# Performance work log

Measured on AMD Instinct MI355X. Metric: run time of the kernel, lower is better.

Reference implementation:

```python
import jax, jax.numpy as jnp
import numpy as np

B, N, E, P, NH = 8, 1024, 768, 768, 12
HD = P // NH


def setup_inputs() -> dict:
    key = jax.random.key(0)
    ks = jax.random.split(key, 9)
    s = lambda k, sh: jax.random.normal(k, sh, dtype=jnp.float32) * 0.02
    return {
        "x": jax.random.normal(ks[0], (B, N, E), dtype=jnp.float32),
        "wq": s(ks[1], (E, P)), "bq": jnp.zeros((P,), jnp.float32),
        "wk": s(ks[2], (E, P)), "bk": jnp.zeros((P,), jnp.float32),
        "wv": s(ks[3], (E, P)), "bv": jnp.zeros((P,), jnp.float32),
        "wo": s(ks[4], (P, E)), "bo": jnp.zeros((E,), jnp.float32),
        "H": 32, "W": 32,
    }


def reference(x, wq, bq, wk, bk, wv, bv, wo, bo, H, W):
    b, n, _ = x.shape
    # QKV projections: [B,N,P] -> [B,NH,N,HD]
    def split_heads(t):
        return t.reshape(b, n, NH, HD).transpose(0, 2, 1, 3)
    q = split_heads(x @ wq + bq)
    k = split_heads(x @ wk + bk)
    v = split_heads(x @ wv + bv)
    # NOTE: original module applies NO 1/sqrt(head_dim) scaling.
    logits = jnp.einsum("bhqd,bhkd->bhqk", q, k)  # [B,NH,N,N]
    attn = jax.nn.softmax(logits, axis=-1)
    ctx = jnp.einsum("bhqk,bhkd->bhqd", attn, v)  # [B,NH,N,HD]
    ctx = ctx.transpose(0, 2, 1, 3).reshape(b, n, P)
    return ctx @ wo + bo
```

## Files before the change

kernel.cpp:

```cpp
#include <hip/hip_runtime.h>
#include <hip/hip_bf16.h>
#include <math.h>

#define B_   8
#define N_   1024
#define E_   768
#define P_   768
#define NH_  12
#define HD_  64

typedef __attribute__((ext_vector_type(8))) short short8;
typedef __attribute__((ext_vector_type(4))) float f32x4;

__device__ inline void async16(void* lds, const void* g) {
    __builtin_amdgcn_global_load_lds(
        (const __attribute__((address_space(1))) void*)g,
        (__attribute__((address_space(3))) void*)lds, 16, 0, 0);
}

__device__ inline unsigned lds_addr(const void* p) {
    return (unsigned)(unsigned long long)(__attribute__((address_space(3))) const char*)p;
}

__device__ inline unsigned pkbf(float a, float b) {
    union { float f; unsigned u; } ua, ub;
    ua.f = a; ub.f = b;
    return __builtin_amdgcn_perm(ub.u, ua.u, 0x07060302u);
}

__global__ __launch_bounds__(256) void cvt_x(const float* __restrict__ x,
                                             __hip_bfloat16* __restrict__ xb, int n4) {
    int i = blockIdx.x * blockDim.x + threadIdx.x;
    const int stride = gridDim.x * blockDim.x;
    for (; i < n4; i += stride) {
        float4 f = ((const float4*)x)[i];
        union { __hip_bfloat16 h[4]; uint2 u; } pk;
        pk.h[0] = __float2bfloat16(f.x);
        pk.h[1] = __float2bfloat16(f.y);
        pk.h[2] = __float2bfloat16(f.z);
        pk.h[3] = __float2bfloat16(f.w);
        ((uint2*)xb)[i] = pk.u;
    }
}

__global__ __launch_bounds__(256) void cvt_tw(
    const float* __restrict__ W0, const float* __restrict__ W1,
    const float* __restrict__ W2, const float* __restrict__ W3,
    __hip_bfloat16* __restrict__ T0, __hip_bfloat16* __restrict__ T1,
    __hip_bfloat16* __restrict__ T2, __hip_bfloat16* __restrict__ T3) {
    const int z = blockIdx.z;
    const float* W = (z == 0) ? W0 : (z == 1) ? W1 : (z == 2) ? W2 : W3;
    __hip_bfloat16* T = (z == 0) ? T0 : (z == 1) ? T1 : (z == 2) ? T2 : T3;
    __shared__ float t[32][33];
    const int tx = threadIdx.x & 31, ty = threadIdx.x >> 5;
    const int n0 = blockIdx.x * 32, k0 = blockIdx.y * 32;
#pragma unroll
    for (int rr = 0; rr < 4; ++rr)
        t[ty + rr * 8][tx] = W[(k0 + ty + rr * 8) * 768 + n0 + tx];
    __syncthreads();
#pragma unroll
    for (int rr = 0; rr < 4; ++rr)
        T[(long)(n0 + ty + rr * 8) * 768 + k0 + tx] = __float2bfloat16(t[tx][ty + rr * 8]);
}

__global__ __launch_bounds__(512, 2) void gemm256(
    const __hip_bfloat16* __restrict__ A0, const __hip_bfloat16* __restrict__ A1,
    const __hip_bfloat16* __restrict__ A2,
    const __hip_bfloat16* __restrict__ B01, const __hip_bfloat16* __restrict__ B2,
    const float* __restrict__ b0, const float* __restrict__ b1,
    const float* __restrict__ b2,
    void* __restrict__ C0, void* __restrict__ C1, void* __restrict__ C2,
    int fused) {
    constexpr int NT = 12;
    __shared__ char L[9 * 16384];

    const __hip_bfloat16* Arows;
    const __hip_bfloat16* Brows;
    const float* bias;
    void* Cout;
    int mode, rb, cb;
    const int xcd = blockIdx.x & 7, t = blockIdx.x >> 3;
    if (fused) {
        const int g = t % 9, yh = t / 9;
        const int y = yh * 8 + xcd;
        if (g < 6) {
            mode = 2;
            const int z = g / 3;
            rb = (g % 3) * 256; cb = y * 256;
            Arows = z ? A1 : A0; Brows = B01; bias = z ? b1 : b0; Cout = z ? C1 : C0;
        } else {
            mode = 1;
            rb = y * 256; cb = (g - 6) * 256;
            Arows = A2; Brows = B2; bias = b2; Cout = C2;
        }
    } else {
        mode = 3;
        const int e3 = t % 3, yh = t / 3;
        const int y = yh * 8 + xcd;
        rb = e3 * 256; cb = y * 256;
        Arows = A0; Brows = B01; bias = b0; Cout = C0;
    }

    const int tid = threadIdx.x;
    const int lane = tid & 63, w = tid >> 6;
    const int wr = w >> 2, wc = w & 3;
    const int l15 = lane & 15, quad = lane >> 4;

    const int rowoff = tid >> 3;
    const int cchunk = (tid & 7) ^ (rowoff & 7);
    const __hip_bfloat16* pA = Arows + (long)(rb + rowoff) * 768 + cchunk * 8;
    const __hip_bfloat16* pB = Brows + (long)(cb + rowoff) * 768 + cchunk * 8;

    const unsigned ldsB = lds_addr(L);

    const int swz = l15 & 7;
    const unsigned lane0 = (unsigned)(l15 * 128 + ((quad ^ swz) << 4));
    const unsigned lane1 = (unsigned)(l15 * 128 + (((4 + quad) ^ swz) << 4));

#define STG(P_, HF_, KT_, SL_)                                                     \
    do {                                                                           \
        const __hip_bfloat16* s_ = (P_) + (HF_) * (128 * 768) + (KT_) * 64;        \
        async16((char*)L + (SL_) * 16384 + tid * 16, s_);                          \
        async16((char*)L + (SL_) * 16384 + 8192 + tid * 16, s_ + 64 * 768);        \
    } while (0)

    STG(pA, 0, 0, 0);
    STG(pB, 0, 0, 1);
    STG(pB, 1, 0, 2);
    STG(pA, 1, 0, 3);
    STG(pA, 0, 1, 4);

    f32x4 acc[8][4];
#pragma unroll
    for (int i = 0; i < 8; ++i)
#pragma unroll
        for (int j = 0; j < 4; ++j) acc[i][j] = (f32x4){0.f, 0.f, 0.f, 0.f};

    int rs = 0;
    int ss = 5;
    const int sAoff = wr ? 3 : 0;
    const int sBoff = (wc < 2) ? 1 : 2;
    const unsigned bColOff = (unsigned)((wc & 1) * 8192);

    for (int kt = 0; kt < NT; ++kt) {
        if (kt < NT - 1) asm volatile("s_waitcnt vmcnt(2)" ::: "memory");
        else             asm volatile("s_waitcnt vmcnt(0)" ::: "memory");
        int sA = rs + sAoff; if (sA >= 9) sA -= 9;
        int sB = rs + sBoff; if (sB >= 9) sB -= 9;
        const unsigned aBase = ldsB + (unsigned)sA * 16384u;
        const unsigned bBase = ldsB + (unsigned)sB * 16384u + bColOff;

        short8 aF[4][2];
#pragma unroll
        for (int s = 0; s < 4; ++s) {
            __builtin_amdgcn_s_barrier();
            asm volatile("" ::: "memory");
            if (4 * kt + 5 + s < 4 * NT) {
                const int ktile = (4 * kt + 5 + s) >> 2;
                if (s == 0)      STG(pB, 0, ktile, ss);
                else if (s == 1) STG(pB, 1, ktile, ss);
                else if (s == 2) STG(pA, 1, ktile, ss);
                else             STG(pA, 0, ktile, ss);
                ++ss; if (ss == 9) ss = 0;
            }

            const int rh = s >> 1, ch = s & 1;
            if ((s & 1) == 0) {
                const unsigned a0 = aBase + (unsigned)(rh * 8192) + lane0;
                const unsigned a1 = aBase + (unsigned)(rh * 8192) + lane1;
#pragma unroll
                for (int rf = 0; rf < 4; ++rf) {
                    asm volatile("ds_read_b128 %0, %1 offset:%2" : "=v"(aF[rf][0]) : "v"(a0), "i"(rf * 2048));
                    asm volatile("ds_read_b128 %0, %1 offset:%2" : "=v"(aF[rf][1]) : "v"(a1), "i"(rf * 2048));
                }
            }
            short8 bF[2][2];
            {
                const unsigned bb0 = bBase + (unsigned)(ch * 4096) + lane0;
                const unsigned bb1 = bBase + (unsigned)(ch * 4096) + lane1;
#pragma unroll
                for (int cf = 0; cf < 2; ++cf) {
                    asm volatile("ds_read_b128 %0, %1 offset:%2" : "=v"(bF[cf][0]) : "v"(bb0), "i"(cf * 2048));
                    asm volatile("ds_read_b128 %0, %1 offset:%2" : "=v"(bF[cf][1]) : "v"(bb1), "i"(cf * 2048));
                }
            }
            asm volatile("s_waitcnt lgkmcnt(0)" ::: "memory");
            __builtin_amdgcn_sched_barrier(0);
            __builtin_amdgcn_s_setprio(1);
#pragma unroll
            for (int rf = 0; rf < 4; ++rf)
#pragma unroll
                for (int cf = 0; cf < 2; ++cf) {
                    acc[rh * 4 + rf][ch * 2 + cf] = __builtin_amdgcn_mfma_f32_16x16x32_bf16(
                        aF[rf][0], bF[cf][0], acc[rh * 4 + rf][ch * 2 + cf], 0, 0, 0);
                    acc[rh * 4 + rf][ch * 2 + cf] = __builtin_amdgcn_mfma_f32_16x16x32_bf16(
                        aF[rf][1], bF[cf][1], acc[rh * 4 + rf][ch * 2 + cf], 0, 0, 0);
                }
            __builtin_amdgcn_s_setprio(0);
        }
        rs += 4; if (rs >= 9) rs -= 9;
    }
#undef STG

    const int eR = rb + wr * 128;
    const int eC = cb + wc * 64;
    if (mode == 2) {
        __hip_bfloat16* O = (__hip_bfloat16*)Cout;
#pragma unroll
        for (int j = 0; j < 4; ++j) {
            const int n = eC + j * 16 + l15;
            const int bb = n >> 10, nn = n & 1023;
#pragma unroll
            for (int i = 0; i < 8; ++i) {
                const int p0 = eR + i * 16 + quad * 4;
                const int h = p0 >> 6, d0 = p0 & 63;
                const float4 bv = *(const float4*)(bias + p0);
                union { __hip_bfloat16 h4[4]; unsigned long long u; } pk;
                pk.h4[0] = __float2bfloat16(acc[i][j][0] + bv.x);
                pk.h4[1] = __float2bfloat16(acc[i][j][1] + bv.y);
                pk.h4[2] = __float2bfloat16(acc[i][j][2] + bv.z);
                pk.h4[3] = __float2bfloat16(acc[i][j][3] + bv.w);
                *(unsigned long long*)(O + (((long)(bb * NH_ + h)) * N_ + nn) * HD_ + d0) = pk.u;
            }
        }
    } else if (mode == 1) {
        __hip_bfloat16* O = (__hip_bfloat16*)Cout;
#pragma unroll
        for (int j = 0; j < 4; ++j) {
            const int p = eC + j * 16 + l15;
            const int h = p >> 6, d = p & 63;
            const float bv = bias[p];
#pragma unroll
            for (int i = 0; i < 8; ++i) {
                const int n0 = eR + i * 16 + quad * 4;
                const int bb = n0 >> 10, nn = n0 & 1023;
                union { __hip_bfloat16 h4[4]; unsigned long long u; } pk;
#pragma unroll
                for (int r = 0; r < 4; ++r)
                    pk.h4[r] = __float2bfloat16(acc[i][j][r] + bv);
                *(unsigned long long*)(O + (((long)(bb * NH_ + h)) * HD_ + d) * N_ + nn) = pk.u;
            }
        }
    } else {
        float* O = (float*)Cout;
#pragma unroll
        for (int j = 0; j < 4; ++j) {
            const int n = eC + j * 16 + l15;
#pragma unroll
            for (int i = 0; i < 8; ++i) {
                const int e0 = eR + i * 16 + quad * 4;
                const float4 bv = *(const float4*)(bias + e0);
                float4 vo;
                vo.x = acc[i][j][0] + bv.x;
                vo.y = acc[i][j][1] + bv.y;
                vo.z = acc[i][j][2] + bv.z;
                vo.w = acc[i][j][3] + bv.w;
                *(float4*)(O + (long)n * 768 + e0) = vo;
            }
        }
    }
}

__global__ __launch_bounds__(256, 3) void attn_mfma(
    const __hip_bfloat16* __restrict__ Q, const __hip_bfloat16* __restrict__ K,
    const __hip_bfloat16* __restrict__ Vt, __hip_bfloat16* __restrict__ ctx) {
    __shared__ __hip_bfloat16 Ks[3 * 64 * 64];
    __shared__ __hip_bfloat16 Vs[3 * 64 * 64];

    const int tid = threadIdx.x;
    const int lane = tid & 63, w = tid >> 6;
    const int l15 = lane & 15, quad = lane >> 4;
    const int y3 = l15 & 7;

    const int bx = blockIdx.x;
    const int rr_ = bx & 7, t_ = bx >> 3;
    const int qb = t_ & 7, hi_ = t_ >> 3;
    const int H = hi_ * 8 + rr_;
    const int bz = H / 12, hy = H - bz * 12;
    const long headOff = (long)H * (N_ * HD_);
    const int qBase = qb * 128;

    short8 qf[2][2];
#pragma unroll
    for (int i = 0; i < 2; ++i)
#pragma unroll
        for (int ks = 0; ks < 2; ++ks)
            qf[i][ks] = *(const short8*)(Q + headOff +
                (long)(qBase + w * 32 + i * 16 + l15) * HD_ + ks * 32 + quad * 8);
    asm volatile("" :: "v"(qf[0][0]), "v"(qf[0][1]), "v"(qf[1][0]), "v"(qf[1][1]));

    f32x4 o[4][2];
#pragma unroll
    for (int mt = 0; mt < 4; ++mt)
#pragma unroll
        for (int i = 0; i < 2; ++i) o[mt][i] = (f32x4){0.f, 0.f, 0.f, 0.f};
    f32x4 ol[2];
    ol[0] = (f32x4){0.f, 0.f, 0.f, 0.f};
    ol[1] = (f32x4){0.f, 0.f, 0.f, 0.f};
    const short8 onesv = (short8){0x3F80, 0x3F80, 0x3F80, 0x3F80,
                                  0x3F80, 0x3F80, 0x3F80, 0x3F80};

    const int p0 = tid, p1 = tid + 256;
    const int r0 = p0 >> 3, lc0 = (p0 & 7) ^ (r0 & 7);
    const int r1 = p1 >> 3, lc1 = (p1 & 7) ^ (r1 & 7);
    const __hip_bfloat16* gK0 = K + headOff + r0 * HD_ + lc0 * 8;
    const __hip_bfloat16* gK1 = K + headOff + r1 * HD_ + lc1 * 8;
    const __hip_bfloat16* gV0 = Vt + headOff + r0 * N_ + lc0 * 8;
    const __hip_bfloat16* gV1 = Vt + headOff + r1 * N_ + lc1 * 8;
    const int q0 = p0 * 16, q1 = p1 * 16;

    const unsigned kfB0 = lds_addr(Ks) + (unsigned)(l15 * 128 + (((0 * 4 + quad) ^ y3) * 16));
    const unsigned kfB1 = lds_addr(Ks) + (unsigned)(l15 * 128 + (((1 * 4 + quad) ^ y3) * 16));
    unsigned vbB[2][2];
#pragma unroll
    for (int g = 0; g < 2; ++g)
#pragma unroll
        for (int h = 0; h < 2; ++h)
            vbB[g][h] = lds_addr(Vs) + (unsigned)(l15 * 128 +
                (((g * 4 + h * 2 + (quad >> 1)) ^ y3) * 16 + (quad & 1) * 8));

    async16((char*)Ks + q0, gK0);
    async16((char*)Ks + q1, gK1);
    async16((char*)Vs + q0, gV0);
    async16((char*)Vs + q1, gV1);
    async16((char*)Ks + 8192 + q0, gK0 + (long)64 * HD_);
    async16((char*)Ks + 8192 + q1, gK1 + (long)64 * HD_);
    async16((char*)Vs + 8192 + q0, gV0 + 64);
    async16((char*)Vs + 8192 + q1, gV1 + 64);

    for (int it = 0; it < 16; ++it) {
        const int bo = (it % 3) * 8192;
        if (it < 15) asm volatile("s_waitcnt vmcnt(4)" ::: "memory");
        else         asm volatile("s_waitcnt vmcnt(0)" ::: "memory");
        __builtin_amdgcn_s_barrier();
        asm volatile("" ::: "memory");
        if (it + 2 < 16) {
            const int po = ((it + 2) % 3) * 8192;
            const long j1 = (long)(it + 2) * 64;
            async16((char*)Ks + po + q0, gK0 + j1 * HD_);
            async16((char*)Ks + po + q1, gK1 + j1 * HD_);
            async16((char*)Vs + po + q0, gV0 + j1);
            async16((char*)Vs + po + q1, gV1 + j1);
        }

        short8 kf[2][4];
        {
            const unsigned ka0 = kfB0 + bo, ka1 = kfB1 + bo;
#pragma unroll
            for (int n = 0; n < 4; ++n)
                asm volatile("ds_read_b128 %0, %1 offset:%2" : "=v"(kf[0][n]) : "v"(ka0), "i"(n * 2048));
#pragma unroll
            for (int n = 0; n < 4; ++n)
                asm volatile("ds_read_b128 %0, %1 offset:%2" : "=v"(kf[1][n]) : "v"(ka1), "i"(n * 2048));
        }
        f32x4 sT[4][2];
#pragma unroll
        for (int n = 0; n < 4; ++n)
#pragma unroll
            for (int i = 0; i < 2; ++i) sT[n][i] = (f32x4){0.f, 0.f, 0.f, 0.f};
        asm volatile("s_waitcnt lgkmcnt(4)" ::: "memory");
        __builtin_amdgcn_sched_barrier(0);
        __builtin_amdgcn_s_setprio(1);
#pragma unroll
        for (int n = 0; n < 4; ++n)
#pragma unroll
            for (int i = 0; i < 2; ++i)
                sT[n][i] = __builtin_amdgcn_mfma_f32_16x16x32_bf16(kf[0][n], qf[i][0], sT[n][i], 0, 0, 0);
        __builtin_amdgcn_s_setprio(0);
        asm volatile("s_waitcnt lgkmcnt(0)" ::: "memory");
        __builtin_amdgcn_sched_barrier(0);
        __builtin_amdgcn_s_setprio(1);
#pragma unroll
        for (int n = 0; n < 4; ++n)
#pragma unroll
            for (int i = 0; i < 2; ++i)
                sT[n][i] = __builtin_amdgcn_mfma_f32_16x16x32_bf16(kf[1][n], qf[i][1], sT[n][i], 0, 0, 0);
        __builtin_amdgcn_s_setprio(0);

        long v0[4][2];
#pragma unroll
        for (int mt = 0; mt < 4; ++mt)
#pragma unroll
            for (int h = 0; h < 2; ++h)
                asm volatile("ds_read_b64 %0, %1 offset:%2" : "=v"(v0[mt][h]) : "v"(vbB[0][h] + bo), "i"(mt * 2048));

        short8 pf[2][2];
#pragma unroll
        for (int i = 0; i < 2; ++i) {
            float pv[4][4];
#pragma unroll
            for (int n = 0; n < 4; ++n)
#pragma unroll
                for (int r = 0; r < 4; ++r)
                    pv[n][r] = __expf(sT[n][i][r] - 16.635532333438686f);
            union { unsigned u[4]; short8 v; } pk0, pk1;
            pk0.u[0] = pkbf(pv[0][0], pv[0][1]);
            pk0.u[1] = pkbf(pv[0][2], pv[0][3]);
            pk0.u[2] = pkbf(pv[1][0], pv[1][1]);
            pk0.u[3] = pkbf(pv[1][2], pv[1][3]);
            pk1.u[0] = pkbf(pv[2][0], pv[2][1]);
            pk1.u[1] = pkbf(pv[2][2], pv[2][3]);
            pk1.u[2] = pkbf(pv[3][0], pv[3][1]);
            pk1.u[3] = pkbf(pv[3][2], pv[3][3]);
            pf[i][0] = pk0.v;
            pf[i][1] = pk1.v;
        }

        asm volatile("s_waitcnt lgkmcnt(0)" ::: "memory");
        __builtin_amdgcn_sched_barrier(0);
        __builtin_amdgcn_s_setprio(1);
#pragma unroll
        for (int mt = 0; mt < 4; ++mt) {
            union { long l[2]; short8 v; } vb;
            vb.l[0] = v0[mt][0]; vb.l[1] = v0[mt][1];
#pragma unroll
            for (int i = 0; i < 2; ++i)
                o[mt][i] = __builtin_amdgcn_mfma_f32_16x16x32_bf16(vb.v, pf[i][0], o[mt][i], 0, 0, 0);
        }
#pragma unroll
        for (int i = 0; i < 2; ++i)
            ol[i] = __builtin_amdgcn_mfma_f32_16x16x32_bf16(onesv, pf[i][0], ol[i], 0, 0, 0);
        __builtin_amdgcn_s_setprio(0);

        long v1[4][2];
#pragma unroll
        for (int mt = 0; mt < 4; ++mt)
#pragma unroll
            for (int h = 0; h < 2; ++h)
                asm volatile("ds_read_b64 %0, %1 offset:%2" : "=v"(v1[mt][h]) : "v"(vbB[1][h] + bo), "i"(mt * 2048));
        asm volatile("s_waitcnt lgkmcnt(0)" ::: "memory");
        __builtin_amdgcn_sched_barrier(0);
        __builtin_amdgcn_s_setprio(1);
#pragma unroll
        for (int mt = 0; mt < 4; ++mt) {
            union { long l[2]; short8 v; } vb;
            vb.l[0] = v1[mt][0]; vb.l[1] = v1[mt][1];
#pragma unroll
            for (int i = 0; i < 2; ++i)
                o[mt][i] = __builtin_amdgcn_mfma_f32_16x16x32_bf16(vb.v, pf[i][1], o[mt][i], 0, 0, 0);
        }
#pragma unroll
        for (int i = 0; i < 2; ++i)
            ol[i] = __builtin_amdgcn_mfma_f32_16x16x32_bf16(onesv, pf[i][1], ol[i], 0, 0, 0);
        __builtin_amdgcn_s_setprio(0);
    }

#pragma unroll
    for (int i = 0; i < 2; ++i) {
        const float inv = 1.0f / ol[i][0];
        const int q = qBase + w * 32 + i * 16 + l15;
        __hip_bfloat16* op = ctx + ((long)(bz * N_ + q)) * P_ + hy * HD_;
#pragma unroll
        for (int mt = 0; mt < 4; ++mt) {
            union { __hip_bfloat16 h[4]; unsigned long long u; } pk;
#pragma unroll
            for (int r = 0; r < 4; ++r)
                pk.h[r] = __float2bfloat16(o[mt][i][r] * inv);
            *(unsigned long long*)(op + mt * 16 + quad * 4) = pk.u;
        }
    }
}

extern "C" void kernel_launch(void* const* d_in, const int* in_sizes, int n_in,
                              void* d_out, int out_size, void* d_ws, size_t ws_size,
                              hipStream_t stream) {
    const float* x  = (const float*)d_in[0];
    const float* wq = (const float*)d_in[1];
    const float* bq = (const float*)d_in[2];
    const float* wk = (const float*)d_in[3];
    const float* bk = (const float*)d_in[4];
    const float* wv = (const float*)d_in[5];
    const float* bv = (const float*)d_in[6];
    const float* wo = (const float*)d_in[7];
    const float* bo = (const float*)d_in[8];
    float* out = (float*)d_out;

    char* p = (char*)d_ws;
    const long XB = (long)B_ * N_ * E_ * 2;
    const long WB = (long)E_ * P_ * 2;
    const long HB = (long)B_ * NH_ * N_ * HD_ * 2;
    __hip_bfloat16* xb  = (__hip_bfloat16*)p; p += XB;
    __hip_bfloat16* wqt = (__hip_bfloat16*)p; p += WB;
    __hip_bfloat16* wkt = (__hip_bfloat16*)p; p += WB;
    __hip_bfloat16* wvt = (__hip_bfloat16*)p; p += WB;
    __hip_bfloat16* wot = (__hip_bfloat16*)p; p += WB;
    __hip_bfloat16* qh  = (__hip_bfloat16*)p; p += HB;
    __hip_bfloat16* kh  = (__hip_bfloat16*)p; p += HB;
    __hip_bfloat16* vth = (__hip_bfloat16*)p; p += HB;
    __hip_bfloat16* ctxb = (__hip_bfloat16*)p; p += HB;

    cvt_x<<<2048, 256, 0, stream>>>(x, xb, (B_ * N_ * E_) / 4);
    cvt_tw<<<dim3(24, 24, 4), 256, 0, stream>>>(wq, wk, wv, wo, wqt, wkt, wvt, wot);

    gemm256<<<dim3(288), 512, 0, stream>>>(
        wqt, wkt, xb, xb, wvt, bq, bk, bv, qh, kh, vth, 1);

    attn_mfma<<<dim3(768), 256, 0, stream>>>(qh, kh, vth, ctxb);

    gemm256<<<dim3(96), 512, 0, stream>>>(
        wot, wot, xb, ctxb, ctxb, bo, bo, bo, out, out, out, 0);
}
```

Measured before the change: 220.6 us.

## Replace fused QKV projection with smaller-tile triple-buffered 128x128 GEMM kernel

Adds a templated gemm_core kernel that uses 128x128 tiles, 256 threads, a K step of 32 and a three-stage async LDS pipeline, and uses it for the fused Q/K/V projection in place of the 256-tile 512-thread gemm256. The grid grows from 288 to 1152 blocks, which improves load balance and occupancy across CUs. In exchange, each tile reuses its operands less and the kernel has more barriers per K step. The output projection still uses gemm256.

```diff
diff --git a/kernel.cpp b/kernel.cpp
--- a/kernel.cpp
+++ b/kernel.cpp
@@ -61,6 +61,181 @@
 #pragma unroll
     for (int rr = 0; rr < 4; ++rr)
         T[(long)(n0 + ty + rr * 8) * 768 + k0 + tx] = __float2bfloat16(t[tx][ty + rr * 8]);
+}
+
+template <int NC>
+__global__ __launch_bounds__(256) void gemm_core(
+    const __hip_bfloat16* __restrict__ A0, const __hip_bfloat16* __restrict__ A1,
+    const __hip_bfloat16* __restrict__ A2,
+    const __hip_bfloat16* __restrict__ B01, const __hip_bfloat16* __restrict__ B2,
+    const float* __restrict__ b0, const float* __restrict__ b1,
+    const float* __restrict__ b2,
+    void* __restrict__ C0, void* __restrict__ C1, void* __restrict__ C2,
+    int fused) {
+    constexpr int ABUF = 8192;
+    constexpr int BBUF = NC * 64;
+    constexpr int JT = NC / 32;
+    __shared__ char As[3 * ABUF];
+    __shared__ char Bs[3 * BBUF];
+
+    const __hip_bfloat16* Arows;
+    const __hip_bfloat16* Brows;
+    const float* bias;
+    void* Cout;
+    int mode, rb, cb;
+    if (fused) {
+        const int xcd = blockIdx.x & 7, t = blockIdx.x >> 3;
+        const int g = t % 18, yhi = t / 18;
+        const int y = yhi * 8 + xcd;
+        if (g < 12) {
+            mode = 2;
+            const int z = g / 6;
+            rb = (g % 6) * 128; cb = y * 128;
+            Arows = z ? A1 : A0; Brows = B01; bias = z ? b1 : b0; Cout = z ? C1 : C0;
+        } else {
+            mode = 1;
+            rb = y * 128; cb = (g - 12) * 128;
+            Arows = A2; Brows = B2; bias = b2; Cout = C2;
+        }
+    } else {
+        mode = 3;
+        const int xcd = blockIdx.x & 7, t = blockIdx.x >> 3;
+        const int e = t % 6, thi = t / 6;
+        const int tc = thi * 8 + xcd;
+        rb = e * 128; cb = tc * NC;
+        Arows = A0; Brows = B01; bias = b0; Cout = C0;
+    }
+
+    const int tid = threadIdx.x;
+    const int lane = tid & 63;
+    const int w = tid >> 6;
+    const int l15 = lane & 15;
+    const int quad = lane >> 4;
+    const int mh = (w >> 1) * 64;
+    const int nh = (w & 1) * (NC / 2);
+
+    f32x4 acc[4][JT];
+#pragma unroll
+    for (int i = 0; i < 4; ++i)
+#pragma unroll
+        for (int j = 0; j < JT; ++j) acc[i][j] = (f32x4){0.f, 0.f, 0.f, 0.f};
+
+    const int c1 = tid + 256;
+    const int ar0 = tid >> 2, alc0 = (tid & 3) ^ ((ar0 >> 1) & 3);
+    const int ar1 = c1 >> 2,  alc1 = (c1 & 3) ^ ((ar1 >> 1) & 3);
+    const __hip_bfloat16* gA0 = Arows + (long)(rb + ar0) * 768 + alc0 * 8;
+    const __hip_bfloat16* gA1 = Arows + (long)(rb + ar1) * 768 + alc1 * 8;
+    const __hip_bfloat16* gB0 = Brows + (long)(cb + ar0) * 768 + alc0 * 8;
+    const __hip_bfloat16* gB1 = (NC == 128) ? (Brows + (long)(cb + ar1) * 768 + alc1 * 8) : nullptr;
+
+    const unsigned aBase0 = lds_addr(As) + (mh + l15) * 64 + ((quad ^ ((l15 >> 1) & 3)) << 4);
+    const unsigned bBase0 = lds_addr(Bs) + (nh + l15) * 64 + ((quad ^ ((l15 >> 1) & 3)) << 4);
+
+    async16(As + tid * 16, gA0);
+    async16(As + c1 * 16, gA1);
+    async16(Bs + tid * 16, gB0);
+    if (NC == 128) async16(Bs + c1 * 16, gB1);
+    async16(As + ABUF + tid * 16, gA0 + 32);
+    async16(As + ABUF + c1 * 16, gA1 + 32);
+    async16(Bs + BBUF + tid * 16, gB0 + 32);
+    if (NC == 128) async16(Bs + BBUF + c1 * 16, gB1 + 32);
+
+    for (int it = 0; it < 24; ++it) {
+        const int bi = it % 3;
+        const int boA = bi * ABUF;
+        const int boB = bi * BBUF;
+        if (it < 23) {
+            if (NC == 128) asm volatile("s_waitcnt vmcnt(4)" ::: "memory");
+            else           asm volatile("s_waitcnt vmcnt(3)" ::: "memory");
+        } else {
+            asm volatile("s_waitcnt vmcnt(0)" ::: "memory");
+        }
+        __builtin_amdgcn_s_barrier();
+        asm volatile("" ::: "memory");
+        if (it + 2 < 24) {
+            const int pb = (it + 2) % 3;
+            const int k2 = (it + 2) * 32;
+            async16(As + pb * ABUF + tid * 16, gA0 + k2);
+            async16(As + pb * ABUF + c1 * 16, gA1 + k2);
+            async16(Bs + pb * BBUF + tid * 16, gB0 + k2);
+            if (NC == 128) async16(Bs + pb * BBUF + c1 * 16, gB1 + k2);
+        }
+
+        const unsigned aB = aBase0 + boA;
+        const unsigned bB = bBase0 + boB;
+        short8 a[4], b[JT];
+#pragma unroll
+        for (int i = 0; i < 4; ++i)
+            asm volatile("ds_read_b128 %0, %1 offset:%2" : "=v"(a[i]) : "v"(aB), "i"(i * 1024));
+#pragma unroll
+        for (int j = 0; j < JT; ++j)
+            asm volatile("ds_read_b128 %0, %1 offset:%2" : "=v"(b[j]) : "v"(bB), "i"(j * 1024));
+        asm volatile("s_waitcnt lgkmcnt(0)" ::: "memory");
+        __builtin_amdgcn_sched_barrier(0);
+        __builtin_amdgcn_s_setprio(1);
+#pragma unroll
+        for (int i = 0; i < 4; ++i)
+#pragma unroll
+            for (int j = 0; j < JT; ++j)
+                acc[i][j] = __builtin_amdgcn_mfma_f32_16x16x32_bf16(a[i], b[j], acc[i][j], 0, 0, 0);
+        __builtin_amdgcn_s_setprio(0);
+    }
+
+    if (mode == 2) {
+        __hip_bfloat16* O = (__hip_bfloat16*)Cout;
+#pragma unroll
+        for (int j = 0; j < JT; ++j) {
+            const int n = cb + nh + j * 16 + l15;
+            const int bb = n >> 10, nn = n & 1023;
+#pragma unroll
+            for (int i = 0; i < 4; ++i) {
+                const int p0 = rb + mh + i * 16 + quad * 4;
+                const int h = p0 >> 6, d0 = p0 & 63;
+                const float4 bv = *(const float4*)(bias + p0);
+                union { __hip_bfloat16 h4[4]; unsigned long long u; } pk;
+                pk.h4[0] = __float2bfloat16(acc[i][j][0] + bv.x);
+                pk.h4[1] = __float2bfloat16(acc[i][j][1] + bv.y);
+                pk.h4[2] = __float2bfloat16(acc[i][j][2] + bv.z);
+                pk.h4[3] = __float2bfloat16(acc[i][j][3] + bv.w);
+                *(unsigned long long*)(O + (((long)(bb * NH_ + h)) * N_ + nn) * HD_ + d0) = pk.u;
+            }
+        }
+    } else if (mode == 1) {
+        __hip_bfloat16* O = (__hip_bfloat16*)Cout;
+#pragma unroll
+        for (int j = 0; j < JT; ++j) {
+            const int p = cb + nh + j * 16 + l15;
+            const int h = p >> 6, d = p & 63;
+            const float bv = bias[p];
+#pragma unroll
+            for (int i = 0; i < 4; ++i) {
+                const int n0 = rb + mh + i * 16 + quad * 4;
+                const int bb = n0 >> 10, nn = n0 & 1023;
+                union { __hip_bfloat16 h4[4]; unsigned long long u; } pk;
+#pragma unroll
+                for (int r = 0; r < 4; ++r)
+                    pk.h4[r] = __float2bfloat16(acc[i][j][r] + bv);
+                *(unsigned long long*)(O + (((long)(bb * NH_ + h)) * HD_ + d) * N_ + nn) = pk.u;
+            }
+        }
+    } else {
+        float* O = (float*)Cout;
+#pragma unroll
+        for (int j = 0; j < JT; ++j) {
+            const int n = cb + nh + j * 16 + l15;
+#pragma unroll
+            for (int i = 0; i < 4; ++i) {
+                const int e0 = rb + mh + i * 16 + quad * 4;
+                const float4 bv = *(const float4*)(bias + e0);
+                float4 vo;
+                vo.x = acc[i][j][0] + bv.x;
+                vo.y = acc[i][j][1] + bv.y;
+                vo.z = acc[i][j][2] + bv.z;
+                vo.w = acc[i][j][3] + bv.w;
+                *(float4*)(O + (long)n * 768 + e0) = vo;
+            }
+        }
+    }
 }
 
 __global__ __launch_bounds__(512, 2) void gemm256(
@@ -492,7 +667,7 @@
     cvt_x<<<2048, 256, 0, stream>>>(x, xb, (B_ * N_ * E_) / 4);
     cvt_tw<<<dim3(24, 24, 4), 256, 0, stream>>>(wq, wk, wv, wo, wqt, wkt, wvt, wot);
 
-    gemm256<<<dim3(288), 512, 0, stream>>>(
+    gemm_core<128><<<dim3(1152), 256, 0, stream>>>(
         wqt, wkt, xb, xb, wvt, bq, bk, bv, qh, kh, vth, 1);
 
     attn_mfma<<<dim3(768), 256, 0, stream>>>(qh, kh, vth, ctxb);
```

New measurement: 212.0 us. 3.9% less time.
